# Kernel optimization log

Hardware: AMD Instinct MI355X
Metric: run time of the kernel (lower is better)

## Reference

```python
import math
import jax, jax.numpy as jnp
import numpy as np

B, S, D, H, P, FF = 64, 100, 768, 8, 8, 3072
HD = D // H
NUM_LAYERS = 4
EPS = 1e-5


def _layernorm(x, g, b):
    m = jnp.mean(x, axis=-1, keepdims=True)
    v = jnp.mean(jnp.square(x - m), axis=-1, keepdims=True)
    return (x - m) * jax.lax.rsqrt(v + EPS) * g + b


def _positional_encoding(seq_len, d_model):
    pos = jnp.arange(seq_len, dtype=jnp.float32)[:, None]
    div = jnp.exp(jnp.arange(0, d_model, 2, dtype=jnp.float32) * (-math.log(10000.0) / d_model))
    pe = jnp.zeros((seq_len, d_model), dtype=jnp.float32)
    pe = pe.at[:, 0::2].set(jnp.sin(pos * div))
    pe = pe.at[:, 1::2].set(jnp.cos(pos * div))
    return pe[None]  # [1, S, D]


def setup_inputs() -> dict:
    key = jax.random.key(0)
    ks = jax.random.split(key, 12)
    s = 0.02
    return {
        "template_seq": jax.random.normal(ks[0], (B, S, D), jnp.float32),
        "param_seq": jax.random.normal(ks[1], (B, S, P, 768), jnp.float32),
        # ParamEncoder (shared across all 4 layers)
        "Wc": jax.random.normal(ks[2], (768, D), jnp.float32) * s,
        "bc": jnp.zeros((D,), jnp.float32),
        "gp": jnp.ones((D,), jnp.float32),
        "bp": jnp.zeros((D,), jnp.float32),
        # FFN (shared)
        "W1": jax.random.normal(ks[3], (D, FF), jnp.float32) * s,
        "b1": jnp.zeros((FF,), jnp.float32),
        "W2": jax.random.normal(ks[4], (FF, D), jnp.float32) * s,
        "b2": jnp.zeros((D,), jnp.float32),
        # LayerNorms (shared)
        "g1": jnp.ones((D,), jnp.float32),
        "bn1": jnp.zeros((D,), jnp.float32),
        "g2": jnp.ones((D,), jnp.float32),
        "bn2": jnp.zeros((D,), jnp.float32),
        # final classifier
        "Wfc": jax.random.normal(ks[5], (D * S, 2), jnp.float32) * s,
        "bfc": jnp.zeros((2,), jnp.float32),
    }


def _layer(src, param_seq, Wc, bc, gp, bp, W1, b1, W2, b2, g1, bn1, g2, bn2):
    inv_sqrt_hd = 1.0 / math.sqrt(HD)
    # ParamEncoder: Linear(768->D) per param vector, mean over params, LayerNorm.
    # Linear is linear => mean-then-project is identical to project-then-mean.
    pooled = jnp.mean(param_seq, axis=2)                  # [B, S, 768]
    param_enc = _layernorm(pooled @ Wc + bc, gp, bp)       # [B, S, D]
    pb = param_enc.reshape(B, S, H, HD).transpose(0, 2, 1, 3)  # [B, H, S, HD]
    param_bias = jnp.einsum('bhqd,bhkd->bhqk', pb, pb) * inv_sqrt_hd
    # attention with q = k = v = src (no projections in the original forward)
    q = src.reshape(B, S, H, HD).transpose(0, 2, 1, 3)     # [B, H, S, HD]
    attn = jnp.einsum('bhqd,bhkd->bhqk', q, q) * inv_sqrt_hd + param_bias
    attn = jax.nn.softmax(attn, axis=-1)
    out = jnp.einsum('bhqk,bhkd->bhqd', attn, q)
    out = out.transpose(0, 2, 1, 3).reshape(B, S, D)
    src = _layernorm(src + out, g1, bn1)
    ffn = jax.nn.gelu(src @ W1 + b1, approximate=False) @ W2 + b2
    return _layernorm(src + ffn, g2, bn2)


def reference(template_seq, param_seq, Wc, bc, gp, bp, W1, b1, W2, b2,
              g1, bn1, g2, bn2, Wfc, bfc):
    x = template_seq + _positional_encoding(S, D)
    for _ in range(NUM_LAYERS):
        x = _layer(x, param_seq, Wc, bc, gp, bp, W1, b1, W2, b2, g1, bn1, g2, bn2)
    return x.reshape(B, S * D) @ Wfc + bfc  # [B, 2]
```

## Files before the change

kernel.cpp:

```cpp
#include <hip/hip_runtime.h>
#include <hip/hip_bf16.h>
#include <math.h>


typedef __attribute__((ext_vector_type(8))) short bf16x8;
typedef __attribute__((ext_vector_type(4))) float f32x4;
typedef __attribute__((ext_vector_type(4))) short short4v;

#define BB 64
#define SS 100
#define DD 768
#define HH 8
#define HD 96
#define FF_ 3072
#define ROWS 6400
#define LN10000 9.210340371976184f

__device__ __forceinline__ void async_copy16(void* lds_dst, const void* gsrc) {
  __builtin_amdgcn_global_load_lds(
      (const __attribute__((address_space(1))) void*)gsrc,
      (__attribute__((address_space(3))) void*)lds_dst, 16, 0, 0);
}

__device__ __forceinline__ float block_sum256(float v, float* sbuf) {
#pragma unroll
  for (int o = 32; o > 0; o >>= 1) v += __shfl_xor(v, o, 64);
  int tid = threadIdx.x;
  __syncthreads();
  if ((tid & 63) == 0) sbuf[tid >> 6] = v;
  __syncthreads();
  return sbuf[0] + sbuf[1] + sbuf[2] + sbuf[3];
}

__device__ __forceinline__ float block_sum192(float v, float* sbuf) {
#pragma unroll
  for (int o = 32; o > 0; o >>= 1) v += __shfl_xor(v, o, 64);
  int tid = threadIdx.x;
  __syncthreads();
  if ((tid & 63) == 0) sbuf[tid >> 6] = v;
  __syncthreads();
  return sbuf[0] + sbuf[1] + sbuf[2];
}

__global__ void convert_transpose(const float* __restrict__ in,
                                  __hip_bfloat16* __restrict__ out,
                                  int K, int N) {
  __shared__ float t[32][33];
  int n0 = blockIdx.x * 32, k0 = blockIdx.y * 32;
  int tid = threadIdx.x;
  int tx = tid & 31, ty = tid >> 5;
#pragma unroll
  for (int j = 0; j < 32; j += 8)
    t[ty + j][tx] = in[(size_t)(k0 + ty + j) * N + n0 + tx];
  __syncthreads();
#pragma unroll
  for (int j = 0; j < 32; j += 8)
    out[(size_t)(n0 + ty + j) * K + k0 + tx] = __float2bfloat16(t[tx][ty + j]);
}

__global__ void pool_mean(const float* __restrict__ ps,
                          __hip_bfloat16* __restrict__ pooled) {
  int idx = blockIdx.x * 256 + threadIdx.x;
  int row = idx / DD, c = idx - row * DD;
  float s = 0.f;
#pragma unroll
  for (int p = 0; p < 8; p++) s += ps[(size_t)(row * 8 + p) * DD + c];
  pooled[idx] = __float2bfloat16(s * 0.125f);
}

__global__ void add_pe(const float* __restrict__ t, float* __restrict__ src) {
  int idx = blockIdx.x * 256 + threadIdx.x;
  int row = idx / DD, c = idx - row * DD;
  int srow = row % SS;
  int c2 = c & ~1;
  float ang = (float)srow * expf((float)c2 * (-LN10000 / (float)DD));
  float pe = (c & 1) ? cosf(ang) : sinf(ang);
  src[idx] = t[idx] + pe;
}

template <bool XB16, bool RESID, bool WB16>
__global__ void ln_row(const float* __restrict__ Xf,
                       const __hip_bfloat16* __restrict__ Xb,
                       const float* __restrict__ R,
                       const float* __restrict__ g, const float* __restrict__ bb,
                       float* __restrict__ of, __hip_bfloat16* __restrict__ ob) {
  int row = blockIdx.x, tid = threadIdx.x;
  size_t base = (size_t)row * DD;
  int c4 = tid * 4;
  float4 v;
  if constexpr (XB16) {
    short4v xv = *(const short4v*)(Xb + base + c4);
    __hip_bfloat16* p = (__hip_bfloat16*)&xv;
    v.x = __bfloat162float(p[0]); v.y = __bfloat162float(p[1]);
    v.z = __bfloat162float(p[2]); v.w = __bfloat162float(p[3]);
  } else {
    v = *(const float4*)(Xf + base + c4);
  }
  if (RESID) {
    float4 rv = *(const float4*)(R + base + c4);
    v.x += rv.x; v.y += rv.y; v.z += rv.z; v.w += rv.w;
  }
  __shared__ float sbuf[3];
  float s = block_sum192(v.x + v.y + v.z + v.w, sbuf);
  float mean = s * (1.0f / DD);
  float dx = v.x - mean, dy = v.y - mean, dz = v.z - mean, dw = v.w - mean;
  float ss = block_sum192(dx * dx + dy * dy + dz * dz + dw * dw, sbuf);
  float rs = rsqrtf(ss * (1.0f / DD) + 1e-5f);
  float4 gv = *(const float4*)(g + c4);
  float4 bv = *(const float4*)(bb + c4);
  float4 y;
  y.x = dx * rs * gv.x + bv.x;
  y.y = dy * rs * gv.y + bv.y;
  y.z = dz * rs * gv.z + bv.z;
  y.w = dw * rs * gv.w + bv.w;
  *(float4*)(of + base + c4) = y;
  if (WB16) {
    __hip_bfloat16 hb[4] = {__float2bfloat16(y.x), __float2bfloat16(y.y),
                            __float2bfloat16(y.z), __float2bfloat16(y.w)};
    *(short4v*)(ob + base + c4) = *(short4v*)hb;
  }
}

__launch_bounds__(256, 2)
__global__ void param_bias_mfma(const float* __restrict__ penc,
                                float* __restrict__ pbias) {
  __shared__ __align__(16) __hip_bfloat16 Qs[128][104];
  const int bh = blockIdx.x;
  const int b = bh >> 3, h = bh & 7;
  const int tid = threadIdx.x;
  const int wave = tid >> 6, lane = tid & 63;
  const int r = lane & 15, quad = lane >> 4;
  const int q8 = quad * 8;
  const int wr = (wave >> 1) * 64, wc = (wave & 1) * 64;
  const float sroot = rsqrtf(9.79795897113f);
  for (int i = tid; i < 128 * HD; i += 256) {
    int s = i / HD, d = i - s * HD;
    float v = (s < SS) ? penc[(size_t)(b * SS + s) * DD + h * HD + d] : 0.f;
    Qs[s][d] = __float2bfloat16(v * sroot);
  }
  __syncthreads();
  f32x4 acc[4][4] = {};
#pragma unroll
  for (int k0 = 0; k0 < HD; k0 += 32) {
    bf16x8 af[4], bfv[4];
#pragma unroll
    for (int mi = 0; mi < 4; mi++)
      af[mi] = *(const bf16x8*)&Qs[wr + mi * 16 + r][k0 + q8];
#pragma unroll
    for (int ni = 0; ni < 4; ni++)
      bfv[ni] = *(const bf16x8*)&Qs[wc + ni * 16 + r][k0 + q8];
#pragma unroll
    for (int mi = 0; mi < 4; mi++)
#pragma unroll
      for (int ni = 0; ni < 4; ni++)
        acc[mi][ni] = __builtin_amdgcn_mfma_f32_16x16x32_bf16(af[mi], bfv[ni],
                                                              acc[mi][ni], 0, 0, 0);
  }
  float* pb = pbias + (size_t)bh * SS * SS;
#pragma unroll
  for (int mi = 0; mi < 4; mi++)
#pragma unroll
    for (int ni = 0; ni < 4; ni++) {
      int col = wc + ni * 16 + r;
      if (col < SS) {
#pragma unroll
        for (int rg = 0; rg < 4; rg++) {
          int row = wr + mi * 16 + quad * 4 + rg;
          if (row < SS) pb[row * SS + col] = acc[mi][ni][rg];
        }
      }
    }
}

__launch_bounds__(256, 2)
__global__ void attn_fused_mfma(const float* __restrict__ src,
                                const float* __restrict__ pbias,
                                __hip_bfloat16* __restrict__ out) {
  __shared__ __align__(16) char umem[128 * 136 * 2];
  __shared__ __align__(16) __hip_bfloat16 Qt[96][136];
  __shared__ float redm[2][128];
  __shared__ float reds[2][128];
  __hip_bfloat16 (*Qs)[104] = (__hip_bfloat16 (*)[104])umem;
  __hip_bfloat16 (*Ps)[136] = (__hip_bfloat16 (*)[136])umem;

  const int bh = blockIdx.x;
  const int b = bh >> 3, h = bh & 7;
  const int tid = threadIdx.x;
  const int wave = tid >> 6, lane = tid & 63;
  const int r = lane & 15, quad = lane >> 4;
  const int q8 = quad * 8;
  const int wr = (wave >> 1) * 64, wc = (wave & 1) * 64;

  const float sroot = rsqrtf(9.79795897113f);
  for (int i = tid; i < SS * HD; i += 256) {
    int s = i / HD, d = i - s * HD;
    float v = src[(size_t)(b * SS + s) * DD + h * HD + d];
    Qs[s][d] = __float2bfloat16(v * sroot);
    Qt[d][s] = __float2bfloat16(v);
  }
  for (int i = tid; i < 28 * HD; i += 256) {
    int s = i / HD, d = i - s * HD;
    Qs[100 + s][d] = __float2bfloat16(0.f);
    Qt[d][100 + s] = __float2bfloat16(0.f);
  }

  const float* pb = pbias + (size_t)bh * SS * SS;
  bool cv[4]; int cols[4];
#pragma unroll
  for (int ni = 0; ni < 4; ni++) { cols[ni] = wc + ni * 16 + r; cv[ni] = cols[ni] < SS; }
  f32x4 acc[4][4];
#pragma unroll
  for (int mi = 0; mi < 4; mi++)
#pragma unroll
    for (int rg = 0; rg < 4; rg++) {
      int row = wr + mi * 16 + quad * 4 + rg;
#pragma unroll
      for (int ni = 0; ni < 4; ni++)
        acc[mi][ni][rg] = (row < SS && cv[ni]) ? pb[row * SS + cols[ni]] : 0.f;
    }
  __syncthreads();

#pragma unroll
  for (int k0 = 0; k0 < HD; k0 += 32) {
    bf16x8 af[4], bfv[4];
#pragma unroll
    for (int mi = 0; mi < 4; mi++)
      af[mi] = *(const bf16x8*)&Qs[wr + mi * 16 + r][k0 + q8];
#pragma unroll
    for (int ni = 0; ni < 4; ni++)
      bfv[ni] = *(const bf16x8*)&Qs[wc + ni * 16 + r][k0 + q8];
#pragma unroll
    for (int mi = 0; mi < 4; mi++)
#pragma unroll
      for (int ni = 0; ni < 4; ni++)
        acc[mi][ni] = __builtin_amdgcn_mfma_f32_16x16x32_bf16(af[mi], bfv[ni],
                                                              acc[mi][ni], 0, 0, 0);
  }

  float mx[4][4];
#pragma unroll
  for (int mi = 0; mi < 4; mi++)
#pragma unroll
    for (int rg = 0; rg < 4; rg++) {
      float m = -1e30f;
#pragma unroll
      for (int ni = 0; ni < 4; ni++)
        if (cv[ni]) m = fmaxf(m, acc[mi][ni][rg]);
#pragma unroll
      for (int o = 1; o < 16; o <<= 1) m = fmaxf(m, __shfl_xor(m, o, 64));
      mx[mi][rg] = m;
    }
  if (r == 0) {
#pragma unroll
    for (int mi = 0; mi < 4; mi++)
#pragma unroll
      for (int rg = 0; rg < 4; rg++)
        redm[wave & 1][wr + mi * 16 + quad * 4 + rg] = mx[mi][rg];
  }
  __syncthreads();

#pragma unroll
  for (int mi = 0; mi < 4; mi++)
#pragma unroll
    for (int rg = 0; rg < 4; rg++) {
      int row = wr + mi * 16 + quad * 4 + rg;
      float rmax = fmaxf(redm[0][row], redm[1][row]);
      float s = 0.f;
#pragma unroll
      for (int ni = 0; ni < 4; ni++) {
        float e = cv[ni] ? __expf(acc[mi][ni][rg] - rmax) : 0.f;
        acc[mi][ni][rg] = e;
        s += e;
      }
#pragma unroll
      for (int o = 1; o < 16; o <<= 1) s += __shfl_xor(s, o, 64);
      if (r == 0) reds[wave & 1][row] = s;
    }
  __syncthreads();

#pragma unroll
  for (int mi = 0; mi < 4; mi++)
#pragma unroll
    for (int rg = 0; rg < 4; rg++) {
      int row = wr + mi * 16 + quad * 4 + rg;
      float inv = 1.0f / (reds[0][row] + reds[1][row]);
#pragma unroll
      for (int ni = 0; ni < 4; ni++)
        Ps[row][cols[ni]] = __float2bfloat16(acc[mi][ni][rg] * inv);
    }
  __syncthreads();

  const int wr2 = (wave >> 1) * 48;
  f32x4 po[3][4] = {};
#pragma unroll
  for (int kk = 0; kk < 128; kk += 32) {
    bf16x8 aq[3], bp[4];
#pragma unroll
    for (int mi = 0; mi < 3; mi++)
      aq[mi] = *(const bf16x8*)&Qt[wr2 + mi * 16 + r][kk + q8];
#pragma unroll
    for (int ni = 0; ni < 4; ni++)
      bp[ni] = *(const bf16x8*)&Ps[wc + ni * 16 + r][kk + q8];
#pragma unroll
    for (int mi = 0; mi < 3; mi++)
#pragma unroll
      for (int ni = 0; ni < 4; ni++)
        po[mi][ni] = __builtin_amdgcn_mfma_f32_16x16x32_bf16(aq[mi], bp[ni],
                                                             po[mi][ni], 0, 0, 0);
  }
#pragma unroll
  for (int mi = 0; mi < 3; mi++)
#pragma unroll
    for (int ni = 0; ni < 4; ni++) {
      int qcol = wc + ni * 16 + r;
      if (qcol < SS) {
        int d0 = wr2 + mi * 16 + quad * 4;
        __hip_bfloat16 hb[4];
#pragma unroll
        for (int rg = 0; rg < 4; rg++) hb[rg] = __float2bfloat16(po[mi][ni][rg]);
        *(short4v*)(out + (size_t)(b * SS + qcol) * DD + h * HD + d0) = *(short4v*)hb;
      }
    }
}

template <int MODE>
__launch_bounds__(256)
__global__ void gemm_bt(const __hip_bfloat16* __restrict__ A,
                        const __hip_bfloat16* __restrict__ Bt,
                        const float* __restrict__ bias,
                        const float* __restrict__ resid,
                        float* __restrict__ outf,
                        __hip_bfloat16* __restrict__ outb,
                        int M, int N, int K) {
  constexpr int BM = 128, BN = 128, BK = 32;
  __shared__ __align__(16) __hip_bfloat16 As[BM * BK];
  __shared__ __align__(16) __hip_bfloat16 Bs[BN * BK];
  const int tid = threadIdx.x;
  const int wave = tid >> 6, lane = tid & 63;
  const int wr = (wave >> 1) * 64, wc = (wave & 1) * 64;
  const int m0 = blockIdx.y * BM, n0 = blockIdx.x * BN;
  const int r = lane & 15, q = lane >> 4;

  f32x4 acc[4][4] = {};

  for (int k0 = 0; k0 < K; k0 += BK) {
#pragma unroll
    for (int j = 0; j < 2; j++) {
      int li = tid + 256 * j;
      int row = li >> 2, cp = li & 3;
      async_copy16(As + li * 8, A + (size_t)(m0 + row) * K + k0 + cp * 8);
      async_copy16(Bs + li * 8, Bt + (size_t)(n0 + row) * K + k0 + cp * 8);
    }
    __syncthreads();
    bf16x8 af[4], bfr[4];
#pragma unroll
    for (int mi = 0; mi < 4; mi++)
      af[mi] = *(const bf16x8*)(As + (wr + mi * 16 + r) * BK + q * 8);
#pragma unroll
    for (int ni = 0; ni < 4; ni++)
      bfr[ni] = *(const bf16x8*)(Bs + (wc + ni * 16 + r) * BK + q * 8);
#pragma unroll
    for (int mi = 0; mi < 4; mi++)
#pragma unroll
      for (int ni = 0; ni < 4; ni++)
        acc[mi][ni] = __builtin_amdgcn_mfma_f32_16x16x32_bf16(af[mi], bfr[ni],
                                                              acc[mi][ni], 0, 0, 0);
    __syncthreads();
  }

#pragma unroll
  for (int mi = 0; mi < 4; mi++) {
#pragma unroll
    for (int ni = 0; ni < 4; ni++) {
      int col = n0 + wc + ni * 16 + r;
      float bv = bias[col];
#pragma unroll
      for (int rg = 0; rg < 4; rg++) {
        int row = m0 + wr + mi * 16 + q * 4 + rg;
        size_t oidx = (size_t)row * N + col;
        float v = acc[mi][ni][rg] + bv;
        if constexpr (MODE == 2) v += resid[oidx];
        if constexpr (MODE == 1) {
          v = 0.5f * v * (1.0f + erff(v * 0.70710678118654752f));
          outb[oidx] = __float2bfloat16(v);
        } else {
          outf[oidx] = v;
        }
      }
    }
  }
}

#define CCHUNK 3072
#define NCHUNK 25
__global__ void classifier_part(const float* __restrict__ x,
                                const float* __restrict__ Wfc,
                                float* __restrict__ part) {
  int chunk = blockIdx.x, b = blockIdx.y, tid = threadIdx.x;
  const float* xb = x + (size_t)b * (SS * DD) + chunk * CCHUNK;
  const float* w = Wfc + 2 * (size_t)chunk * CCHUNK;
  float a0 = 0.f, a1 = 0.f;
  for (int i = tid; i < CCHUNK; i += 256) {
    float xv = xb[i];
    float2 wv = *(const float2*)(w + 2 * i);
    a0 += xv * wv.x;
    a1 += xv * wv.y;
  }
  __shared__ float sbuf[4];
  a0 = block_sum256(a0, sbuf);
  a1 = block_sum256(a1, sbuf);
  if (tid == 0) {
    part[(b * NCHUNK + chunk) * 2] = a0;
    part[(b * NCHUNK + chunk) * 2 + 1] = a1;
  }
}

__global__ void classifier_final(const float* __restrict__ part,
                                 const float* __restrict__ bfc,
                                 float* __restrict__ out) {
  int b = threadIdx.x;
  float a0 = bfc[0], a1 = bfc[1];
#pragma unroll
  for (int c = 0; c < NCHUNK; c++) {
    a0 += part[(b * NCHUNK + c) * 2];
    a1 += part[(b * NCHUNK + c) * 2 + 1];
  }
  out[2 * b] = a0;
  out[2 * b + 1] = a1;
}

extern "C" void kernel_launch(void* const* d_in, const int* in_sizes, int n_in,
                              void* d_out, int out_size, void* d_ws, size_t ws_size,
                              hipStream_t stream) {
  const float* Tmpl = (const float*)d_in[0];
  const float* Pseq = (const float*)d_in[1];
  const float* Wc   = (const float*)d_in[2];
  const float* bc   = (const float*)d_in[3];
  const float* gp   = (const float*)d_in[4];
  const float* bp   = (const float*)d_in[5];
  const float* W1   = (const float*)d_in[6];
  const float* b1   = (const float*)d_in[7];
  const float* W2   = (const float*)d_in[8];
  const float* b2   = (const float*)d_in[9];
  const float* g1   = (const float*)d_in[10];
  const float* bn1  = (const float*)d_in[11];
  const float* g2   = (const float*)d_in[12];
  const float* bn2  = (const float*)d_in[13];
  const float* Wfc  = (const float*)d_in[14];
  const float* bfc  = (const float*)d_in[15];
  float* out = (float*)d_out;
  (void)in_sizes; (void)n_in; (void)out_size; (void)ws_size;

  char* ws = (char*)d_ws;
  size_t off = 0;
  auto alloc = [&](size_t n) { size_t o = off; off += (n + 255) & ~(size_t)255; return o; };

  __hip_bfloat16* Wct = (__hip_bfloat16*)(ws + alloc((size_t)768 * 768 * 2));
  __hip_bfloat16* W1t = (__hip_bfloat16*)(ws + alloc((size_t)768 * 3072 * 2));
  __hip_bfloat16* W2t = (__hip_bfloat16*)(ws + alloc((size_t)3072 * 768 * 2));
  size_t h1_off = alloc((size_t)ROWS * FF_ * 2);
  __hip_bfloat16* h1 = (__hip_bfloat16*)(ws + h1_off);
  float* param_enc = (float*)(ws + h1_off);
  size_t slb_off = alloc((size_t)ROWS * DD * 2);
  __hip_bfloat16* src_ln_bf = (__hip_bfloat16*)(ws + slb_off);
  __hip_bfloat16* pooled = (__hip_bfloat16*)(ws + slb_off);
  size_t ao_off = alloc((size_t)ROWS * DD * 4);
  __hip_bfloat16* attn_out_b = (__hip_bfloat16*)(ws + ao_off);
  float* pe_lin = (float*)(ws + ao_off);
  float* pbias = (float*)(ws + alloc((size_t)512 * SS * SS * 4));
  float* src = (float*)(ws + alloc((size_t)ROWS * DD * 4));
  float* src_ln = (float*)(ws + alloc((size_t)ROWS * DD * 4));
  float* z = (float*)(ws + alloc((size_t)ROWS * DD * 4));
  float* cpart = (float*)(ws + alloc((size_t)BB * NCHUNK * 2 * 4));

  convert_transpose<<<dim3(768 / 32, 768 / 32), 256, 0, stream>>>(Wc, Wct, 768, 768);
  convert_transpose<<<dim3(3072 / 32, 768 / 32), 256, 0, stream>>>(W1, W1t, 768, 3072);
  convert_transpose<<<dim3(768 / 32, 3072 / 32), 256, 0, stream>>>(W2, W2t, 3072, 768);
  pool_mean<<<ROWS * DD / 256, 256, 0, stream>>>(Pseq, pooled);
  gemm_bt<0><<<dim3(DD / 128, ROWS / 128), 256, 0, stream>>>(
      pooled, Wct, bc, nullptr, pe_lin, nullptr, ROWS, DD, 768);
  ln_row<false, false, false><<<ROWS, 192, 0, stream>>>(
      pe_lin, nullptr, nullptr, gp, bp, param_enc, nullptr);
  param_bias_mfma<<<512, 256, 0, stream>>>(param_enc, pbias);
  add_pe<<<ROWS * DD / 256, 256, 0, stream>>>(Tmpl, src);

  for (int l = 0; l < 4; ++l) {
    attn_fused_mfma<<<512, 256, 0, stream>>>(src, pbias, attn_out_b);
    ln_row<true, true, true><<<ROWS, 192, 0, stream>>>(
        nullptr, attn_out_b, src, g1, bn1, src_ln, src_ln_bf);
    gemm_bt<1><<<dim3(FF_ / 128, ROWS / 128), 256, 0, stream>>>(
        src_ln_bf, W1t, b1, nullptr, nullptr, h1, ROWS, FF_, DD);
    gemm_bt<2><<<dim3(DD / 128, ROWS / 128), 256, 0, stream>>>(
        h1, W2t, b2, src_ln, z, nullptr, ROWS, DD, FF_);
    ln_row<false, false, false><<<ROWS, 192, 0, stream>>>(
        z, nullptr, nullptr, g2, bn2, src, nullptr);
  }

  classifier_part<<<dim3(NCHUNK, BB), 256, 0, stream>>>(src, Wfc, cpart);
  classifier_final<<<1, 64, 0, stream>>>(cpart, bfc, out);
}
```

Before: 1.079 ms.

## Double-buffer GEMM LDS tiles and XOR-swizzle layout to avoid bank conflicts

The bf16 MFMA GEMM now keeps two LDS buffers per operand and issues the async global-to-LDS copies for the next K tile before computing on the current one, so load latency can overlap with MFMA work. Only one barrier per iteration remains. It also XOR-swizzles the 16-byte chunk position within each row, keyed on row bits, to cut LDS bank conflicts on the fragment reads. This doubles LDS use per block, which may lower occupancy, and the single barrier assumes the async copies are complete by the time it is reached.

Result: no change. 1.075 ms (-0.4%).

```diff
diff --git a/kernel.cpp b/kernel.cpp
--- a/kernel.cpp
+++ b/kernel.cpp
@@ -333,40 +333,60 @@
                         __hip_bfloat16* __restrict__ outb,
                         int M, int N, int K) {
   constexpr int BM = 128, BN = 128, BK = 32;
-  __shared__ __align__(16) __hip_bfloat16 As[BM * BK];
-  __shared__ __align__(16) __hip_bfloat16 Bs[BN * BK];
+  __shared__ __align__(16) __hip_bfloat16 As[2][BM * BK];
+  __shared__ __align__(16) __hip_bfloat16 Bs[2][BN * BK];
   const int tid = threadIdx.x;
   const int wave = tid >> 6, lane = tid & 63;
   const int wr = (wave >> 1) * 64, wc = (wave & 1) * 64;
   const int m0 = blockIdx.y * BM, n0 = blockIdx.x * BN;
   const int r = lane & 15, q = lane >> 4;
+  const int q8 = q * 8;
+  const int key8 = ((r >> 1) & 3) * 8;
+
+  const int liA = tid, liB = tid + 256;
+  const int rowA = liA >> 2, rowB = liB >> 2;
+  const int cpA = (liA & 3) ^ ((rowA >> 1) & 3);
+  const int cpB = (liB & 3) ^ ((rowB >> 1) & 3);
+  const __hip_bfloat16* gA0 = A + (size_t)(m0 + rowA) * K + cpA * 8;
+  const __hip_bfloat16* gA1 = A + (size_t)(m0 + rowB) * K + cpB * 8;
+  const __hip_bfloat16* gB0 = Bt + (size_t)(n0 + rowA) * K + cpA * 8;
+  const __hip_bfloat16* gB1 = Bt + (size_t)(n0 + rowB) * K + cpB * 8;
 
   f32x4 acc[4][4] = {};
 
-  for (int k0 = 0; k0 < K; k0 += BK) {
-#pragma unroll
-    for (int j = 0; j < 2; j++) {
-      int li = tid + 256 * j;
-      int row = li >> 2, cp = li & 3;
-      async_copy16(As + li * 8, A + (size_t)(m0 + row) * K + k0 + cp * 8);
-      async_copy16(Bs + li * 8, Bt + (size_t)(n0 + row) * K + k0 + cp * 8);
-    }
-    __syncthreads();
+  auto stage = [&](int buf, int k0) {
+    async_copy16(&As[buf][liA * 8], gA0 + k0);
+    async_copy16(&As[buf][liB * 8], gA1 + k0);
+    async_copy16(&Bs[buf][liA * 8], gB0 + k0);
+    async_copy16(&Bs[buf][liB * 8], gB1 + k0);
+  };
+  auto compute = [&](int buf) {
     bf16x8 af[4], bfr[4];
 #pragma unroll
     for (int mi = 0; mi < 4; mi++)
-      af[mi] = *(const bf16x8*)(As + (wr + mi * 16 + r) * BK + q * 8);
+      af[mi] = *(const bf16x8*)(&As[buf][(wr + mi * 16 + r) * BK + (q8 ^ key8)]);
 #pragma unroll
     for (int ni = 0; ni < 4; ni++)
-      bfr[ni] = *(const bf16x8*)(Bs + (wc + ni * 16 + r) * BK + q * 8);
+      bfr[ni] = *(const bf16x8*)(&Bs[buf][(wc + ni * 16 + r) * BK + (q8 ^ key8)]);
 #pragma unroll
     for (int mi = 0; mi < 4; mi++)
 #pragma unroll
       for (int ni = 0; ni < 4; ni++)
         acc[mi][ni] = __builtin_amdgcn_mfma_f32_16x16x32_bf16(af[mi], bfr[ni],
                                                               acc[mi][ni], 0, 0, 0);
+  };
+
+  const int NT = K / BK;
+  stage(0, 0);
+  __syncthreads();
+  int cur = 0;
+  for (int t = 0; t < NT - 1; ++t) {
+    stage(cur ^ 1, (t + 1) * BK);
+    compute(cur);
     __syncthreads();
-  }
+    cur ^= 1;
+  }
+  compute(cur);
 
 #pragma unroll
   for (int mi = 0; mi < 4; mi++) {
```

## Replace GEMM with 256x128 triple-buffered pipelined kernel and XCD-aware tile mapping

Applied to the files above, without the earlier changes.

Replaces the single-buffered 128x128x32 GEMM with a 256x128x64, 512-thread kernel. It uses a 3-stage LDS ring of async global-to-LDS copies spread across two half-steps and an XOR-swizzled LDS layout to avoid bank conflicts. It also adds a block-index remap that keeps consecutive tiles on the same XCD, plus setprio around the MFMA bursts. The goal is to hide global load latency, cut barriers per FLOP and improve L2 locality, at the cost of more LDS (144KB) and fewer blocks for the N=768 GEMMs (150 workgroups).

Measured after the change: 984.2 us. 1.1x faster.

```diff
diff --git a/kernel.cpp b/kernel.cpp
--- a/kernel.cpp
+++ b/kernel.cpp
@@ -324,59 +324,131 @@
 }
 
 template <int MODE>
-__launch_bounds__(256)
-__global__ void gemm_bt(const __hip_bfloat16* __restrict__ A,
+__launch_bounds__(512, 2)
+__global__ void gemm256(const __hip_bfloat16* __restrict__ A,
                         const __hip_bfloat16* __restrict__ Bt,
                         const float* __restrict__ bias,
                         const float* __restrict__ resid,
                         float* __restrict__ outf,
                         __hip_bfloat16* __restrict__ outb,
                         int M, int N, int K) {
-  constexpr int BM = 128, BN = 128, BK = 32;
-  __shared__ __align__(16) __hip_bfloat16 As[BM * BK];
-  __shared__ __align__(16) __hip_bfloat16 Bs[BN * BK];
+  constexpr int BM = 256, BN = 128, BK = 64;
+  __shared__ __align__(16) __hip_bfloat16 As[3][BM * BK];
+  __shared__ __align__(16) __hip_bfloat16 Bs[3][BN * BK];
+  const int gm = M >> 8, gn = N >> 7;
+  const int nwg = gm * gn;
+  int wg = (int)blockIdx.x;
+  {
+    int qc = nwg >> 3, rc = nwg & 7;
+    int xcd = wg & 7, pos = wg >> 3;
+    wg = (xcd < rc ? xcd * (qc + 1) : rc * (qc + 1) + (xcd - rc) * qc) + pos;
+  }
+  const int nt0 = wg / gm, mt = wg - nt0 * gm;
+  const int m0 = mt * BM, n0 = nt0 * BN;
   const int tid = threadIdx.x;
   const int wave = tid >> 6, lane = tid & 63;
-  const int wr = (wave >> 1) * 64, wc = (wave & 1) * 64;
-  const int m0 = blockIdx.y * BM, n0 = blockIdx.x * BN;
+  const int wm = wave >> 1, wn = wave & 1;
   const int r = lane & 15, q = lane >> 4;
 
+  const int srow = tid >> 3;
+  const int scp = (tid & 7) ^ ((tid >> 4) & 7);
+  const __hip_bfloat16* gA0 = A + (size_t)(m0 + srow) * K + scp * 8;
+  const __hip_bfloat16* gA1 = A + (size_t)(m0 + srow + 64) * K + scp * 8;
+  const __hip_bfloat16* gA2 = A + (size_t)(m0 + srow + 128) * K + scp * 8;
+  const __hip_bfloat16* gA3 = A + (size_t)(m0 + srow + 192) * K + scp * 8;
+  const __hip_bfloat16* gB0 = Bt + (size_t)(n0 + srow) * K + scp * 8;
+  const __hip_bfloat16* gB1 = Bt + (size_t)(n0 + srow + 64) * K + scp * 8;
+
+  const int kr = (r >> 1) & 7;
+  const int c0 = (q ^ kr) * 8;
+  const int c1 = ((4 + q) ^ kr) * 8;
+  const int aBase = wm * 4096 + r * 64;
+  const int bBase = wn * 4096 + r * 64;
+
   f32x4 acc[4][4] = {};
 
-  for (int k0 = 0; k0 < K; k0 += BK) {
-#pragma unroll
-    for (int j = 0; j < 2; j++) {
-      int li = tid + 256 * j;
-      int row = li >> 2, cp = li & 3;
-      async_copy16(As + li * 8, A + (size_t)(m0 + row) * K + k0 + cp * 8);
-      async_copy16(Bs + li * 8, Bt + (size_t)(n0 + row) * K + k0 + cp * 8);
-    }
-    __syncthreads();
-    bf16x8 af[4], bfr[4];
-#pragma unroll
-    for (int mi = 0; mi < 4; mi++)
-      af[mi] = *(const bf16x8*)(As + (wr + mi * 16 + r) * BK + q * 8);
-#pragma unroll
-    for (int ni = 0; ni < 4; ni++)
-      bfr[ni] = *(const bf16x8*)(Bs + (wc + ni * 16 + r) * BK + q * 8);
-#pragma unroll
-    for (int mi = 0; mi < 4; mi++)
-#pragma unroll
-      for (int ni = 0; ni < 4; ni++)
-        acc[mi][ni] = __builtin_amdgcn_mfma_f32_16x16x32_bf16(af[mi], bfr[ni],
-                                                              acc[mi][ni], 0, 0, 0);
-    __syncthreads();
+  const int NT = K / BK;
+#pragma unroll
+  for (int t = 0; t < 2; ++t) {
+    const int kel = t * BK;
+    async_copy16(&As[t][tid * 8],          gA0 + kel);
+    async_copy16(&As[t][(tid + 512) * 8],  gA1 + kel);
+    async_copy16(&As[t][(tid + 1024) * 8], gA2 + kel);
+    async_copy16(&As[t][(tid + 1536) * 8], gA3 + kel);
+    async_copy16(&Bs[t][tid * 8],          gB0 + kel);
+    async_copy16(&Bs[t][(tid + 512) * 8],  gB1 + kel);
+  }
+  asm volatile("s_waitcnt vmcnt(6)" ::: "memory");
+  __builtin_amdgcn_s_barrier();
+  __builtin_amdgcn_sched_barrier(0);
+
+  int slot = 0;
+  for (int t = 0; t < NT; ++t) {
+    const int s2 = (slot >= 1) ? slot - 1 : slot + 2;
+    const bool st = (t + 2 < NT);
+    const int kel = (t + 2) * BK;
+    {
+      bf16x8 af[4], bfr[4];
+#pragma unroll
+      for (int mi = 0; mi < 4; mi++)
+        af[mi] = *(const bf16x8*)(&As[slot][aBase + mi * 1024 + c0]);
+#pragma unroll
+      for (int ni = 0; ni < 4; ni++)
+        bfr[ni] = *(const bf16x8*)(&Bs[slot][bBase + ni * 1024 + c0]);
+      if (st) {
+        async_copy16(&As[s2][tid * 8],         gA0 + kel);
+        async_copy16(&As[s2][(tid + 512) * 8], gA1 + kel);
+        async_copy16(&Bs[s2][tid * 8],         gB0 + kel);
+      }
+      __builtin_amdgcn_s_setprio(1);
+#pragma unroll
+      for (int mi = 0; mi < 4; mi++)
+#pragma unroll
+        for (int ni = 0; ni < 4; ni++)
+          acc[mi][ni] = __builtin_amdgcn_mfma_f32_16x16x32_bf16(af[mi], bfr[ni],
+                                                                acc[mi][ni], 0, 0, 0);
+      __builtin_amdgcn_s_setprio(0);
+      __builtin_amdgcn_s_barrier();
+      __builtin_amdgcn_sched_barrier(0);
+    }
+    {
+      bf16x8 af[4], bfr[4];
+#pragma unroll
+      for (int mi = 0; mi < 4; mi++)
+        af[mi] = *(const bf16x8*)(&As[slot][aBase + mi * 1024 + c1]);
+#pragma unroll
+      for (int ni = 0; ni < 4; ni++)
+        bfr[ni] = *(const bf16x8*)(&Bs[slot][bBase + ni * 1024 + c1]);
+      if (st) {
+        async_copy16(&As[s2][(tid + 1024) * 8], gA2 + kel);
+        async_copy16(&As[s2][(tid + 1536) * 8], gA3 + kel);
+        async_copy16(&Bs[s2][(tid + 512) * 8],  gB1 + kel);
+      }
+      __builtin_amdgcn_s_setprio(1);
+#pragma unroll
+      for (int mi = 0; mi < 4; mi++)
+#pragma unroll
+        for (int ni = 0; ni < 4; ni++)
+          acc[mi][ni] = __builtin_amdgcn_mfma_f32_16x16x32_bf16(af[mi], bfr[ni],
+                                                                acc[mi][ni], 0, 0, 0);
+      __builtin_amdgcn_s_setprio(0);
+      if (st) asm volatile("s_waitcnt vmcnt(6)" ::: "memory");
+      else    asm volatile("s_waitcnt vmcnt(0)" ::: "memory");
+      __builtin_amdgcn_s_barrier();
+      __builtin_amdgcn_sched_barrier(0);
+    }
+    slot = (slot == 2) ? 0 : slot + 1;
   }
 
 #pragma unroll
   for (int mi = 0; mi < 4; mi++) {
 #pragma unroll
     for (int ni = 0; ni < 4; ni++) {
-      int col = n0 + wc + ni * 16 + r;
+      int col = n0 + wn * 64 + ni * 16 + r;
       float bv = bias[col];
 #pragma unroll
       for (int rg = 0; rg < 4; rg++) {
-        int row = m0 + wr + mi * 16 + q * 4 + rg;
+        int row = m0 + wm * 64 + mi * 16 + q * 4 + rg;
         size_t oidx = (size_t)row * N + col;
         float v = acc[mi][ni][rg] + bv;
         if constexpr (MODE == 2) v += resid[oidx];
@@ -477,7 +549,7 @@
   convert_transpose<<<dim3(3072 / 32, 768 / 32), 256, 0, stream>>>(W1, W1t, 768, 3072);
   convert_transpose<<<dim3(768 / 32, 3072 / 32), 256, 0, stream>>>(W2, W2t, 3072, 768);
   pool_mean<<<ROWS * DD / 256, 256, 0, stream>>>(Pseq, pooled);
-  gemm_bt<0><<<dim3(DD / 128, ROWS / 128), 256, 0, stream>>>(
+  gemm256<0><<<(DD / 128) * (ROWS / 256), 512, 0, stream>>>(
       pooled, Wct, bc, nullptr, pe_lin, nullptr, ROWS, DD, 768);
   ln_row<false, false, false><<<ROWS, 192, 0, stream>>>(
       pe_lin, nullptr, nullptr, gp, bp, param_enc, nullptr);
@@ -488,9 +560,9 @@
     attn_fused_mfma<<<512, 256, 0, stream>>>(src, pbias, attn_out_b);
     ln_row<true, true, true><<<ROWS, 192, 0, stream>>>(
         nullptr, attn_out_b, src, g1, bn1, src_ln, src_ln_bf);
-    gemm_bt<1><<<dim3(FF_ / 128, ROWS / 128), 256, 0, stream>>>(
+    gemm256<1><<<(FF_ / 128) * (ROWS / 256), 512, 0, stream>>>(
         src_ln_bf, W1t, b1, nullptr, nullptr, h1, ROWS, FF_, DD);
-    gemm_bt<2><<<dim3(DD / 128, ROWS / 128), 256, 0, stream>>>(
+    gemm256<2><<<(DD / 128) * (ROWS / 256), 512, 0, stream>>>(
         h1, W2t, b2, src_ln, z, nullptr, ROWS, DD, FF_);
     ln_row<false, false, false><<<ROWS, 192, 0, stream>>>(
         z, nullptr, nullptr, g2, bn2, src, nullptr);
```
